# Optimization experiments

Measured on AMD Instinct MI355X. Metric: run time of the kernel, lower is better.

## Reference

```python
import jax, jax.numpy as jnp
import numpy as np

N = 50000      # num_nodes
R = 32         # num_relations
H = 16         # hidden channels
C = 16         # num_classes
E = 1600000    # num_edges (avg degree 32)


def setup_inputs() -> dict:
    key = jax.random.key(0)
    ks = jax.random.split(key, 8)
    edge_index = jax.random.randint(ks[0], (2, E), 0, N)
    edge_type = jnp.sort(jax.random.randint(ks[1], (E,), 0, R))
    # per-relation [start, end) slices into the sorted edge list (is_sorted=True)
    starts = jnp.searchsorted(edge_type, jnp.arange(R))
    ends = jnp.searchsorted(edge_type, jnp.arange(R) + 1)
    tensor_slice = jnp.stack([starts, ends], axis=1)
    s = 0.05
    W1 = jax.random.normal(ks[2], (R, N, H), dtype=jnp.float32) * s   # layer-1 per-relation embedding (x=None)
    root1 = jax.random.normal(ks[3], (N, H), dtype=jnp.float32) * s  # root weight acts as embedding when x=None
    bias1 = jax.random.normal(ks[4], (H,), dtype=jnp.float32) * s
    W2 = jax.random.normal(ks[5], (R, H, C), dtype=jnp.float32) * s
    root2 = jax.random.normal(ks[6], (H, C), dtype=jnp.float32) * s
    bias2 = jax.random.normal(ks[7], (C,), dtype=jnp.float32) * s
    return {"edge_index": edge_index, "edge_type": edge_type, "tensor_slice": tensor_slice,
            "W1": W1, "root1": root1, "bias1": bias1,
            "W2": W2, "root2": root2, "bias2": bias2}


def reference(edge_index, edge_type, tensor_slice, W1, root1, bias1, W2, root2, bias2):
    src, dst = edge_index[0], edge_index[1]
    # ---- layer 1: x=None, so per-relation transform is an embedding lookup W1[r][src]
    msg1 = W1[edge_type, src]                                        # [E, H] relation-indexed gather
    h1 = root1 + jax.ops.segment_sum(msg1, dst, num_segments=N) + bias1
    h1 = jax.nn.relu(h1)
    # ---- layer 2: transform all nodes per relation once, then gather per edge
    t = jnp.einsum('nh,rhc->rnc', h1, W2)                            # [R, N, C]
    msg2 = t[edge_type, src]                                         # [E, C]
    h2 = h1 @ root2 + jax.ops.segment_sum(msg2, dst, num_segments=N) + bias2
    return jax.nn.log_softmax(h2, axis=1)
```

## Files before the change

kernel.cpp:

```cpp
#include <hip/hip_runtime.h>

static constexpr int H  = 16;
static constexpr int C  = 16;

__global__ void k1_scatter(const int* __restrict__ srcv, const int* __restrict__ dstv,
                           const int* __restrict__ etv, const float* __restrict__ W1,
                           float* __restrict__ acc1, int E, int N) {
    int t = blockIdx.x * blockDim.x + threadIdx.x;
    if (t >= E * 16) return;
    int e = t >> 4;
    int c = t & 15;
    int s = srcv[e];
    int d = dstv[e];
    int r = etv[e];
    float v = W1[((size_t)r * N + (size_t)s) * H + c];
    unsafeAtomicAdd(acc1 + (size_t)d * H + c, v);
}

__global__ void k2_fin1(const float* __restrict__ root1, const float* __restrict__ bias1,
                        const float* __restrict__ acc1, float* __restrict__ h1, int total4) {
    int i = blockIdx.x * blockDim.x + threadIdx.x;
    if (i >= total4) return;
    float4 rv = ((const float4*)root1)[i];
    float4 av = ((const float4*)acc1)[i];
    float4 bv = ((const float4*)bias1)[i & 3];
    float4 o;
    o.x = fmaxf(rv.x + av.x + bv.x, 0.0f);
    o.y = fmaxf(rv.y + av.y + bv.y, 0.0f);
    o.z = fmaxf(rv.z + av.z + bv.z, 0.0f);
    o.w = fmaxf(rv.w + av.w + bv.w, 0.0f);
    ((float4*)h1)[i] = o;
}

__global__ void k3_scatter(const int* __restrict__ srcv, const int* __restrict__ dstv,
                           const int* __restrict__ etv, const float* __restrict__ h1,
                           const float* __restrict__ W2, float* __restrict__ out, int E) {
    int t = blockIdx.x * blockDim.x + threadIdx.x;
    if (t >= E * 16) return;
    int e = t >> 4;
    int c = t & 15;
    int s = srcv[e];
    int d = dstv[e];
    int r = etv[e];
    const float4* hr = (const float4*)(h1 + (size_t)s * H);
    float4 h0 = hr[0], h1v = hr[1], h2v = hr[2], h3v = hr[3];
    const float* w = W2 + (size_t)r * H * C + c;
    float acc = 0.f;
    acc += h0.x * w[0 * C];  acc += h0.y * w[1 * C];
    acc += h0.z * w[2 * C];  acc += h0.w * w[3 * C];
    acc += h1v.x * w[4 * C]; acc += h1v.y * w[5 * C];
    acc += h1v.z * w[6 * C]; acc += h1v.w * w[7 * C];
    acc += h2v.x * w[8 * C]; acc += h2v.y * w[9 * C];
    acc += h2v.z * w[10 * C]; acc += h2v.w * w[11 * C];
    acc += h3v.x * w[12 * C]; acc += h3v.y * w[13 * C];
    acc += h3v.z * w[14 * C]; acc += h3v.w * w[15 * C];
    unsafeAtomicAdd(out + (size_t)d * C + c, acc);
}

__global__ void k4_fin2(const float* __restrict__ h1, const float* __restrict__ root2,
                        const float* __restrict__ bias2, float* __restrict__ out, int N) {
    int n = blockIdx.x * blockDim.x + threadIdx.x;
    if (n >= N) return;
    const float* hr = h1 + (size_t)n * H;
    float h[16];
#pragma unroll
    for (int k = 0; k < 16; ++k) h[k] = hr[k];
    float* o = out + (size_t)n * C;
    float z[16];
#pragma unroll
    for (int c = 0; c < 16; ++c) {
        float acc = o[c] + bias2[c];
#pragma unroll
        for (int k = 0; k < 16; ++k) acc += h[k] * root2[k * C + c];
        z[c] = acc;
    }
    float m = z[0];
#pragma unroll
    for (int c = 1; c < 16; ++c) m = fmaxf(m, z[c]);
    float se = 0.f;
#pragma unroll
    for (int c = 0; c < 16; ++c) se += __expf(z[c] - m);
    float lse = m + __logf(se);
#pragma unroll
    for (int c = 0; c < 16; ++c) o[c] = z[c] - lse;
}

extern "C" void kernel_launch(void* const* d_in, const int* in_sizes, int n_in,
                              void* d_out, int out_size, void* d_ws, size_t ws_size,
                              hipStream_t stream) {
    const int*   edge_index = (const int*)d_in[0];
    const int*   edge_type  = (const int*)d_in[1];
    const float* W1    = (const float*)d_in[3];
    const float* root1 = (const float*)d_in[4];
    const float* bias1 = (const float*)d_in[5];
    const float* W2    = (const float*)d_in[6];
    const float* root2 = (const float*)d_in[7];
    const float* bias2 = (const float*)d_in[8];
    float* out = (float*)d_out;

    const int E = in_sizes[0] / 2;
    const int N = in_sizes[4] / H;
    const int* srcv = edge_index;
    const int* dstv = edge_index + E;

    float* acc1 = (float*)d_ws;
    float* h1   = acc1 + (size_t)N * H;

    hipMemsetAsync(acc1, 0, (size_t)N * H * sizeof(float), stream);
    hipMemsetAsync(out, 0, (size_t)out_size * sizeof(float), stream);

    const int B = 256;
    int t16 = E * 16;
    k1_scatter<<<(t16 + B - 1) / B, B, 0, stream>>>(srcv, dstv, edge_type, W1, acc1, E, N);
    int total4 = N * H / 4;
    k2_fin1<<<(total4 + B - 1) / B, B, 0, stream>>>(root1, bias1, acc1, h1, total4);
    k3_scatter<<<(t16 + B - 1) / B, B, 0, stream>>>(srcv, dstv, edge_type, h1, W2, out, E);
    k4_fin2<<<(N + B - 1) / B, B, 0, stream>>>(h1, root2, bias2, out, N);
}
```

Baseline: 216.4 us.

## Replace atomic edge scatter with per-call CSR build and destination-gather kernels

```diff
diff --git a/kernel.cpp b/kernel.cpp
--- a/kernel.cpp
+++ b/kernel.cpp
@@ -1,95 +1,145 @@
 #include <hip/hip_runtime.h>
+#include <hip/hip_bf16.h>
 
-static constexpr int H  = 16;
-static constexpr int C  = 16;
+static constexpr int H = 16;
+static constexpr int C = 16;
 
-__global__ void k1_scatter(const int* __restrict__ srcv, const int* __restrict__ dstv,
-                           const int* __restrict__ etv, const float* __restrict__ W1,
-                           float* __restrict__ acc1, int E, int N) {
-    int t = blockIdx.x * blockDim.x + threadIdx.x;
-    if (t >= E * 16) return;
-    int e = t >> 4;
-    int c = t & 15;
-    int s = srcv[e];
-    int d = dstv[e];
-    int r = etv[e];
-    float v = W1[((size_t)r * N + (size_t)s) * H + c];
-    unsafeAtomicAdd(acc1 + (size_t)d * H + c, v);
+static __device__ inline unsigned short f2bf(float x) {
+    __hip_bfloat16 b = __float2bfloat16(x);
+    return *reinterpret_cast<unsigned short*>(&b);
+}
+static __device__ inline float bflo(unsigned u) { return __uint_as_float(u << 16); }
+static __device__ inline float bfhi(unsigned u) { return __uint_as_float(u & 0xffff0000u); }
+
+__global__ void k_deg(const int* __restrict__ dstv, int* __restrict__ deg, int E) {
+    int e = blockIdx.x * blockDim.x + threadIdx.x;
+    if (e < E) atomicAdd(&deg[dstv[e]], 1);
 }
 
-__global__ void k2_fin1(const float* __restrict__ root1, const float* __restrict__ bias1,
-                        const float* __restrict__ acc1, float* __restrict__ h1, int total4) {
-    int i = blockIdx.x * blockDim.x + threadIdx.x;
-    if (i >= total4) return;
-    float4 rv = ((const float4*)root1)[i];
-    float4 av = ((const float4*)acc1)[i];
-    float4 bv = ((const float4*)bias1)[i & 3];
-    float4 o;
-    o.x = fmaxf(rv.x + av.x + bv.x, 0.0f);
-    o.y = fmaxf(rv.y + av.y + bv.y, 0.0f);
-    o.z = fmaxf(rv.z + av.z + bv.z, 0.0f);
-    o.w = fmaxf(rv.w + av.w + bv.w, 0.0f);
-    ((float4*)h1)[i] = o;
+__global__ void k_scan1(const int* __restrict__ deg, int* __restrict__ cursor,
+                        int* __restrict__ bsum, int N) {
+    __shared__ int sh[256];
+    int tid = threadIdx.x;
+    int base = blockIdx.x * 1024 + tid * 4;
+    int d0 = (base + 0 < N) ? deg[base + 0] : 0;
+    int d1 = (base + 1 < N) ? deg[base + 1] : 0;
+    int d2 = (base + 2 < N) ? deg[base + 2] : 0;
+    int d3 = (base + 3 < N) ? deg[base + 3] : 0;
+    int t = d0 + d1 + d2 + d3;
+    sh[tid] = t;
+    __syncthreads();
+    for (int off = 1; off < 256; off <<= 1) {
+        int v = (tid >= off) ? sh[tid - off] : 0;
+        __syncthreads();
+        sh[tid] += v;
+        __syncthreads();
+    }
+    int excl = sh[tid] - t;
+    if (tid == 255) bsum[blockIdx.x] = sh[255];
+    int run = excl;
+    if (base + 0 < N) { cursor[base + 0] = run; run += d0; }
+    if (base + 1 < N) { cursor[base + 1] = run; run += d1; }
+    if (base + 2 < N) { cursor[base + 2] = run; run += d2; }
+    if (base + 3 < N) { cursor[base + 3] = run; run += d3; }
 }
 
-__global__ void k3_scatter(const int* __restrict__ srcv, const int* __restrict__ dstv,
-                           const int* __restrict__ etv, const float* __restrict__ h1,
-                           const float* __restrict__ W2, float* __restrict__ out, int E) {
-    int t = blockIdx.x * blockDim.x + threadIdx.x;
-    if (t >= E * 16) return;
-    int e = t >> 4;
-    int c = t & 15;
-    int s = srcv[e];
-    int d = dstv[e];
-    int r = etv[e];
-    const float4* hr = (const float4*)(h1 + (size_t)s * H);
-    float4 h0 = hr[0], h1v = hr[1], h2v = hr[2], h3v = hr[3];
-    const float* w = W2 + (size_t)r * H * C + c;
-    float acc = 0.f;
-    acc += h0.x * w[0 * C];  acc += h0.y * w[1 * C];
-    acc += h0.z * w[2 * C];  acc += h0.w * w[3 * C];
-    acc += h1v.x * w[4 * C]; acc += h1v.y * w[5 * C];
-    acc += h1v.z * w[6 * C]; acc += h1v.w * w[7 * C];
-    acc += h2v.x * w[8 * C]; acc += h2v.y * w[9 * C];
-    acc += h2v.z * w[10 * C]; acc += h2v.w * w[11 * C];
-    acc += h3v.x * w[12 * C]; acc += h3v.y * w[13 * C];
-    acc += h3v.z * w[14 * C]; acc += h3v.w * w[15 * C];
-    unsafeAtomicAdd(out + (size_t)d * C + c, acc);
+__global__ void k_scan2(const int* __restrict__ bsum, int* __restrict__ bbase, int nb) {
+    if (threadIdx.x == 0 && blockIdx.x == 0) {
+        int acc = 0;
+        for (int i = 0; i < nb; ++i) { bbase[i] = acc; acc += bsum[i]; }
+    }
 }
 
-__global__ void k4_fin2(const float* __restrict__ h1, const float* __restrict__ root2,
-                        const float* __restrict__ bias2, float* __restrict__ out, int N) {
-    int n = blockIdx.x * blockDim.x + threadIdx.x;
-    if (n >= N) return;
-    const float* hr = h1 + (size_t)n * H;
-    float h[16];
-#pragma unroll
-    for (int k = 0; k < 16; ++k) h[k] = hr[k];
-    float* o = out + (size_t)n * C;
-    float z[16];
-#pragma unroll
-    for (int c = 0; c < 16; ++c) {
-        float acc = o[c] + bias2[c];
-#pragma unroll
-        for (int k = 0; k < 16; ++k) acc += h[k] * root2[k * C + c];
-        z[c] = acc;
+__global__ void k_scan3(int* __restrict__ cursor, const int* __restrict__ bbase, int N) {
+    int i = blockIdx.x * blockDim.x + threadIdx.x;
+    if (i < N) cursor[i] += bbase[i >> 10];
+}
+
+__global__ void k_fill(const int* __restrict__ srcv, const int* __restrict__ dstv,
+                       const int* __restrict__ etv, int* __restrict__ cursor,
+                       unsigned* __restrict__ csr, int E) {
+    int e = blockIdx.x * blockDim.x + threadIdx.x;
+    if (e >= E) return;
+    int d = dstv[e];
+    int pos = atomicAdd(&cursor[d], 1);
+    csr[pos] = ((unsigned)etv[e] << 17) | (unsigned)srcv[e];
+}
+
+__global__ void k0_cast(const float* __restrict__ W2, const float* __restrict__ root2,
+                        unsigned short* __restrict__ w2t, int R) {
+    int i = blockIdx.x * blockDim.x + threadIdx.x;
+    if (i >= (R + 1) * 256) return;
+    int r = i >> 8;
+    int kc = i & 255;
+    int k = kc >> 4, c = kc & 15;
+    float v = (r < R) ? W2[(size_t)r * 256 + k * 16 + c] : root2[k * 16 + c];
+    w2t[(r << 8) + (c << 4) + k] = f2bf(v);
+}
+
+__global__ void k1_csr(const unsigned* __restrict__ csr, const int* __restrict__ cursor,
+                       const int* __restrict__ deg, const float* __restrict__ W1,
+                       const float* __restrict__ root1, const float* __restrict__ bias1,
+                       unsigned short* __restrict__ h1bf, int N) {
+    int t = blockIdx.x * blockDim.x + threadIdx.x;
+    int d = t >> 4, c = t & 15;
+    if (d >= N) return;
+    int end = cursor[d];
+    int start = end - deg[d];
+    float acc = root1[(size_t)d * 16 + c] + bias1[c];
+    for (int i = start; i < end; ++i) {
+        unsigned u = csr[i];
+        int s = u & 0x1ffff;
+        int r = u >> 17;
+        acc += W1[((size_t)r * N + s) * 16 + c];
     }
-    float m = z[0];
-#pragma unroll
-    for (int c = 1; c < 16; ++c) m = fmaxf(m, z[c]);
-    float se = 0.f;
-#pragma unroll
-    for (int c = 0; c < 16; ++c) se += __expf(z[c] - m);
-    float lse = m + __logf(se);
-#pragma unroll
-    for (int c = 0; c < 16; ++c) o[c] = z[c] - lse;
+    h1bf[(size_t)d * 16 + c] = f2bf(fmaxf(acc, 0.f));
+}
+
+__global__ void k3_csr(const unsigned* __restrict__ csr, const int* __restrict__ cursor,
+                       const int* __restrict__ deg, const unsigned short* __restrict__ h1bf,
+                       const unsigned short* __restrict__ w2t, const float* __restrict__ bias2,
+                       float* __restrict__ out, int N, int R) {
+    int t = blockIdx.x * blockDim.x + threadIdx.x;
+    int d = t >> 4, c = t & 15;
+    if (d >= N) return;
+    int end = cursor[d];
+    int start = end - deg[d];
+    float acc = bias2[c];
+    for (int i = start; i <= end; ++i) {
+        int s, r;
+        if (i < end) {
+            unsigned u = csr[i];
+            s = (int)(u & 0x1ffff);
+            r = (int)(u >> 17);
+        } else {
+            s = d; r = R;
+        }
+        const uint4* hp = (const uint4*)(h1bf + (size_t)s * 16);
+        uint4 hlo = hp[0], hhi = hp[1];
+        const uint4* wp = (const uint4*)(w2t + ((size_t)r << 8) + (c << 4));
+        uint4 wlo = wp[0], whi = wp[1];
+        acc += bflo(hlo.x) * bflo(wlo.x) + bfhi(hlo.x) * bfhi(wlo.x);
+        acc += bflo(hlo.y) * bflo(wlo.y) + bfhi(hlo.y) * bfhi(wlo.y);
+        acc += bflo(hlo.z) * bflo(wlo.z) + bfhi(hlo.z) * bfhi(wlo.z);
+        acc += bflo(hlo.w) * bflo(wlo.w) + bfhi(hlo.w) * bfhi(wlo.w);
+        acc += bflo(hhi.x) * bflo(whi.x) + bfhi(hhi.x) * bfhi(whi.x);
+        acc += bflo(hhi.y) * bflo(whi.y) + bfhi(hhi.y) * bfhi(whi.y);
+        acc += bflo(hhi.z) * bflo(whi.z) + bfhi(hhi.z) * bfhi(whi.z);
+        acc += bflo(hhi.w) * bflo(whi.w) + bfhi(hhi.w) * bfhi(whi.w);
+    }
+    float m = acc;
+    for (int off = 8; off; off >>= 1) m = fmaxf(m, __shfl_xor(m, off, 16));
+    float ex = __expf(acc - m);
+    float se = ex;
+    for (int off = 8; off; off >>= 1) se += __shfl_xor(se, off, 16);
+    out[(size_t)d * 16 + c] = acc - m - __logf(se);
 }
 
 extern "C" void kernel_launch(void* const* d_in, const int* in_sizes, int n_in,
                               void* d_out, int out_size, void* d_ws, size_t ws_size,
                               hipStream_t stream) {
-    const int*   edge_index = (const int*)d_in[0];
-    const int*   edge_type  = (const int*)d_in[1];
+    const int*   edge_index   = (const int*)d_in[0];
+    const int*   edge_type    = (const int*)d_in[1];
     const float* W1    = (const float*)d_in[3];
     const float* root1 = (const float*)d_in[4];
     const float* bias1 = (const float*)d_in[5];
@@ -100,20 +150,32 @@
 
     const int E = in_sizes[0] / 2;
     const int N = in_sizes[4] / H;
+    const int R = in_sizes[2] / 2;
     const int* srcv = edge_index;
     const int* dstv = edge_index + E;
 
-    float* acc1 = (float*)d_ws;
-    float* h1   = acc1 + (size_t)N * H;
-
-    hipMemsetAsync(acc1, 0, (size_t)N * H * sizeof(float), stream);
-    hipMemsetAsync(out, 0, (size_t)out_size * sizeof(float), stream);
+    char* p = (char*)d_ws;
+    unsigned* csr = (unsigned*)p;                 p += (size_t)E * 4;
+    unsigned short* h1bf = (unsigned short*)p;    p += (size_t)N * 16 * 2;
+    unsigned short* w2t = (unsigned short*)p;     p += (size_t)(R + 1) * 256 * 2;
+    p = (char*)(((uintptr_t)p + 15) & ~(uintptr_t)15);
+    int* deg = (int*)p;                           p += (size_t)N * 4;
+    int* cursor = (int*)p;                        p += (size_t)N * 4;
+    int* bsum = (int*)p;                          p += 256 * 4;
+    int* bbase = (int*)p;
 
     const int B = 256;
-    int t16 = E * 16;
-    k1_scatter<<<(t16 + B - 1) / B, B, 0, stream>>>(srcv, dstv, edge_type, W1, acc1, E, N);
-    int total4 = N * H / 4;
-    k2_fin1<<<(total4 + B - 1) / B, B, 0, stream>>>(root1, bias1, acc1, h1, total4);
-    k3_scatter<<<(t16 + B - 1) / B, B, 0, stream>>>(srcv, dstv, edge_type, h1, W2, out, E);
-    k4_fin2<<<(N + B - 1) / B, B, 0, stream>>>(h1, root2, bias2, out, N);
+    const int nb = (N + 1023) / 1024;
+
+    hipMemsetAsync(deg, 0, (size_t)N * sizeof(int), stream);
+    k_deg<<<(E + B - 1) / B, B, 0, stream>>>(dstv, deg, E);
+    k_scan1<<<nb, B, 0, stream>>>(deg, cursor, bsum, N);
+    k_scan2<<<1, 64, 0, stream>>>(bsum, bbase, nb);
+    k_scan3<<<(N + B - 1) / B, B, 0, stream>>>(cursor, bbase, N);
+    k_fill<<<(E + B - 1) / B, B, 0, stream>>>(srcv, dstv, edge_type, cursor, csr, E);
+    k0_cast<<<((R + 1) * 256 + B - 1) / B, B, 0, stream>>>(W2, root2, w2t, R);
+
+    int tN = N * 16;
+    k1_csr<<<(tN + B - 1) / B, B, 0, stream>>>(csr, cursor, deg, W1, root1, bias1, h1bf, N);
+    k3_csr<<<(tN + B - 1) / B, B, 0, stream>>>(csr, cursor, deg, h1bf, w2t, bias2, out, N, R);
 }
```

Measured after the change: 341.1 us. 1.58x slower.
